# Kernel tuning notes

Hardware: AMD Instinct MI355X
Metric: run time of the kernel (lower is better)

## Reference

```python
import jax, jax.numpy as jnp
import numpy as np

NEG_SLOPE = 0.2  # PyG GATv2 default negative_slope


def _gru_last(x, W_ih, W_hh, b_ih, b_hh):
    """x: [B, T, Hin] -> final GRU hidden state [B, H] (torch nn.GRU equations)."""
    gx = x @ W_ih.T + b_ih  # [B, T, 3H], input gates precomputed
    H = W_hh.shape[1]

    def step(h, g):
        gh = h @ W_hh.T + b_hh
        xr, xz, xn = jnp.split(g, 3, axis=-1)
        hr, hz, hn = jnp.split(gh, 3, axis=-1)
        r = jax.nn.sigmoid(xr + hr)
        z = jax.nn.sigmoid(xz + hz)
        n = jnp.tanh(xn + r * hn)
        return (1.0 - z) * n + z * h, None

    h0 = jnp.zeros((x.shape[0], H), x.dtype)
    hT, _ = jax.lax.scan(step, h0, jnp.swapaxes(gx, 0, 1))
    return hT


def _conv(x, w, b, stride):
    y = jax.lax.conv_general_dilated(x, w, (stride, stride), 'SAME',
                                     dimension_numbers=('NCHW', 'OIHW', 'NCHW'))
    return jax.nn.relu(y + b[None, :, None, None])


def _forward(obs, phase, obs_map, edges, edges_feature, params):
    (W_nbrs, b_nbrs, W_ih, W_hh, b_ih, b_hh, Wl, Wr, att_a, gat_bias,
     conv1_w, conv1_b, conv2_w, conv2_b, Wc, bc, Wp, bp, Wh, bh,
     Wo, bo, Wa, ba) = params
    B, N = obs.shape[0], obs.shape[1]
    BN = B * N
    heads, C = att_a.shape

    # per-node obs embedding (MLP) + GRU over seq -> last hidden
    x = jax.nn.relu(obs.reshape(BN, obs.shape[2], obs.shape[3]) @ W_nbrs + b_nbrs)
    h = _gru_last(x, W_ih, W_hh, b_ih, b_hh)  # [BN, hidden]

    # flat_edges: offset each sample's node ids by b*N, concat along edge dim
    offsets = (jnp.arange(B) * N)[:, None, None]
    ei = (edges + offsets).transpose(1, 0, 2).reshape(2, -1)  # [2, B*E]
    loops = jnp.arange(BN)  # PyG GATv2 add_self_loops=True
    src = jnp.concatenate([ei[0], loops])
    dst = jnp.concatenate([ei[1], loops])

    # GATv2Conv (heads, concat=False): gather -> leakyrelu -> edge softmax -> scatter
    xl = (h @ Wl).reshape(BN, heads, C)
    xr = (h @ Wr).reshape(BN, heads, C)
    e = jax.nn.leaky_relu(xl[src] + xr[dst], NEG_SLOPE)  # [Etot, heads, C]
    logits = jnp.einsum('ehc,hc->eh', e, att_a)          # [Etot, heads]
    m = jax.ops.segment_max(logits, dst, num_segments=BN)
    p = jnp.exp(logits - m[dst])
    s = jax.ops.segment_sum(p, dst, num_segments=BN)
    alpha = p / s[dst]                                    # [Etot, heads]
    node_out = jax.ops.segment_sum(xl[src] * alpha[..., None], dst, num_segments=BN)
    obs_gat = node_out.mean(axis=1) + gat_bias            # concat=False -> head mean

    source_idx = jnp.arange(B) * N  # ego intersection of each sample
    obs_gat = obs_gat[source_idx]   # [B, hidden]

    # CNNBase on map
    c = _conv(obs_map, conv1_w, conv1_b, 2)
    c = _conv(c, conv2_w, conv2_b, 2)
    target_emb = jax.nn.relu(c.reshape(B, -1) @ Wc + bc)

    # phase MLP, fusion MLP, dueling head
    phase_emb = jax.nn.relu(phase @ Wp + bp)
    fused = jnp.concatenate([obs_gat, target_emb, phase_emb], axis=1)
    hid = jax.nn.relu(fused @ Wh + bh)
    v = hid @ Wo + bo
    adv = hid @ Wa + ba
    out = v + (adv - adv.mean(axis=-1, keepdims=True))
    return out, alpha


def setup_inputs() -> dict:
    key = jax.random.key(0)
    B, N, T, Fo = 16, 1000, 16, 16      # batch, n_nodes, seq_len, obs_length+4
    H, heads, P, A, E = 128, 5, 8, 8, 4000
    Cm, HW = 4, 32
    ks = iter(jax.random.split(key, 40))

    def rn(shape, scale=0.05):
        return jax.random.normal(next(ks), shape, dtype=jnp.float32) * scale

    return dict(
        obs=rn((B, N, T, Fo), 1.0),
        phase=rn((B, P), 1.0),
        obs_map=rn((B, Cm, HW, HW), 1.0),
        edges=jax.random.randint(next(ks), (B, 2, E), 0, N),
        edges_feature=rn((B, E, 4), 1.0),
        W_nbrs=rn((Fo, H)), b_nbrs=jnp.zeros((H,), jnp.float32),
        W_ih=rn((3 * H, H)), W_hh=rn((3 * H, H)),
        b_ih=jnp.zeros((3 * H,), jnp.float32), b_hh=jnp.zeros((3 * H,), jnp.float32),
        Wl=rn((H, heads * H)), Wr=rn((H, heads * H)),
        att_a=rn((heads, H)), gat_bias=jnp.zeros((H,), jnp.float32),
        conv1_w=rn((32, Cm, 3, 3)), conv1_b=jnp.zeros((32,), jnp.float32),
        conv2_w=rn((64, 32, 3, 3)), conv2_b=jnp.zeros((64,), jnp.float32),
        Wc=rn((64 * (HW // 4) * (HW // 4), H)), bc=jnp.zeros((H,), jnp.float32),
        Wp=rn((P, P)), bp=jnp.zeros((P,), jnp.float32),
        Wh=rn((2 * H + P, H)), bh=jnp.zeros((H,), jnp.float32),
        Wo=rn((H, 1)), bo=jnp.zeros((1,), jnp.float32),
        Wa=rn((H, A)), ba=jnp.zeros((A,), jnp.float32),
    )


def reference(obs, phase, obs_map, edges, edges_feature,
              W_nbrs, b_nbrs, W_ih, W_hh, b_ih, b_hh,
              Wl, Wr, att_a, gat_bias,
              conv1_w, conv1_b, conv2_w, conv2_b, Wc, bc,
              Wp, bp, Wh, bh, Wo, bo, Wa, ba):
    params = (W_nbrs, b_nbrs, W_ih, W_hh, b_ih, b_hh, Wl, Wr, att_a, gat_bias,
              conv1_w, conv1_b, conv2_w, conv2_b, Wc, bc, Wp, bp, Wh, bh,
              Wo, bo, Wa, ba)
    return _forward(obs, phase, obs_map, edges, edges_feature, params)
```

## Files before the change

### kernel.cpp

```cpp
#include <hip/hip_runtime.h>
#include <hip/hip_bf16.h>
#include <math.h>

#define B_    16
#define N_    1000
#define BN_   16000
#define T_    16
#define FO    16
#define H_    128
#define G3    384
#define HEADS 5
#define HC    640
#define E_    4000
#define EG    64000
#define ETOT  80000
#define P_    8
#define A_    8
#define NEG_SLOPE 0.2f

typedef __attribute__((ext_vector_type(8))) short bf16x8;
typedef __attribute__((ext_vector_type(4))) float f32x4;

__device__ __forceinline__ float bf2f(unsigned short u){ return __uint_as_float(((unsigned)u)<<16); }
__device__ __forceinline__ unsigned short f2bf(float x){
    unsigned u = __float_as_uint(x);
    unsigned r = (u + 0x7FFFu + ((u>>16)&1u)) >> 16;
    return (unsigned short)r;
}
__device__ __forceinline__ unsigned cvtpk(float lo, float hi){
    unsigned r;
    asm volatile("v_cvt_pk_bf16_f32 %0, %1, %2" : "=v"(r) : "v"(lo), "v"(hi));
    return r;
}
__device__ __forceinline__ float rcpf(float x){ return __builtin_amdgcn_rcpf(x); }

__global__ __launch_bounds__(256) void k_prep_c1(
        const float* __restrict__ Wih, const float* __restrict__ Whh,
        const float* __restrict__ Wl, const float* __restrict__ Wr,
        const float* __restrict__ Wn, const float* __restrict__ bn,
        unsigned short* __restrict__ Wihb, unsigned short* __restrict__ Whhb,
        unsigned short* __restrict__ WTb, unsigned short* __restrict__ WnTb,
        float* __restrict__ segsum, float* __restrict__ node_out,
        float* __restrict__ tacc,
        const float* __restrict__ im, const float* __restrict__ w1,
        const float* __restrict__ b1, float* __restrict__ c1out){
    __shared__ float sW[32*4*9];
    int t = threadIdx.x;
    if(blockIdx.x < 640){
        int i = blockIdx.x*256 + t;
        if(i < G3*H_){ Wihb[i] = f2bf(Wih[i]); Whhb[i] = f2bf(Whh[i]); }
        if(i < 2*HC*H_){
            int c = i >> 7, k = i & 127;
            float v = (c < HC) ? Wl[(size_t)k*HC + c] : Wr[(size_t)k*HC + (c-HC)];
            WTb[i] = f2bf(v);
        }
        if(i < H_*32){
            int c = i >> 5, k = i & 31;
            WnTb[i] = (k < FO) ? f2bf(Wn[k*H_ + c])
                     : (k == FO ? f2bf(bn[c]) : (unsigned short)0);
        }
        if(i < BN_*HEADS) segsum[i] = 0.0f;
        if(i < B_*HC) node_out[i] = 0.0f;
        if(i < B_*H_) tacc[i] = 0.0f;
    } else {
        for(int i=t;i<32*4*9;i+=256) sW[i]=w1[i];
        __syncthreads();
        int idx = (blockIdx.x-640)*256 + t;
        int ox = idx & 15, oy = (idx>>4)&15, oc = (idx>>8)&31, b = idx>>13;
        float acc = b1[oc];
        for(int ic=0;ic<4;ic++){
            const float* ip = &im[(size_t)((b*4+ic)*32)*32];
            const float* wp = &sW[(oc*4+ic)*9];
            #pragma unroll
            for(int ky=0;ky<3;ky++){
                int iy = oy*2+ky; if(iy>=32) continue;
                #pragma unroll
                for(int kx=0;kx<3;kx++){
                    int ix = ox*2+kx; if(ix>=32) continue;
                    acc = fmaf(ip[iy*32+ix], wp[ky*3+kx], acc);
                }
            }
        }
        c1out[idx] = fmaxf(acc, 0.f);
    }
}

__global__ __launch_bounds__(512,2) void k_gruf(const float* __restrict__ obs,
        const unsigned short* __restrict__ WnTb,
        const unsigned short* __restrict__ Wihb, const float* __restrict__ bih,
        const unsigned short* __restrict__ Whhb, const float* __restrict__ bhh,
        unsigned short* __restrict__ hout){
    __shared__ unsigned short sX[2*8192];
    __shared__ unsigned short sH[2*8192];
    int t = threadIdx.x;
    int w = t>>6, lane = t&63, lq = lane>>4, lm = lane&15;

    bf16x8 wfi[3][4], wfh[3][4];
    #pragma unroll
    for(int i=0;i<3;i++){
        int row = (8*i + w)*16 + lm;
        #pragma unroll
        for(int kt=0;kt<4;kt++){
            wfi[i][kt] = *(const bf16x8*)&Wihb[row*H_ + kt*32 + lq*8];
            wfh[i][kt] = *(const bf16x8*)&Whhb[row*H_ + kt*32 + lq*8];
        }
    }
    bf16x8 wfn = *(const bf16x8*)&WnTb[(w*16+lm)*32 + lq*8];
    int cb = w*16 + lq*4;
    f32x4 b_r, b_z, bxn, bhn;
    { f32x4 t1=*(const f32x4*)&bih[cb],     t2=*(const f32x4*)&bhh[cb];     b_r=t1+t2; }
    { f32x4 t1=*(const f32x4*)&bih[128+cb], t2=*(const f32x4*)&bhh[128+cb]; b_z=t1+t2; }
    bxn = *(const f32x4*)&bih[256+cb];
    bhn = *(const f32x4*)&bhh[256+cb];

    int rd[4];
    #pragma unroll
    for(int kt=0;kt<4;kt++) rd[kt] = lm*128 + (((4*kt+lq)^(lm&7))<<3);
    const int wrt = lm*128 + (((2*w + (lq>>1))^(lm&7))<<3) + ((lq&1)<<2);

    int nodeBase = blockIdx.x*64;
    const float* obp0 = &obs[(size_t)(nodeBase + lm)*256 + lq*8];

    for(int i=t;i<4096;i+=512) ((unsigned*)sH)[i] = 0u;
    float ho[4][4] = {{0.f,0.f,0.f,0.f},{0.f,0.f,0.f,0.f},
                      {0.f,0.f,0.f,0.f},{0.f,0.f,0.f,0.f}};

    float4 oA[4], oB[4];
    if(lq < 2){
        #pragma unroll
        for(int g=0; g<4; g++){
            const float* q = obp0 + (size_t)g*16*256;
            oA[g] = *(const float4*)(q);    oB[g] = *(const float4*)(q+4);
        }
    }
    #pragma unroll
    for(int g=0; g<4; g++){
        bf16x8 ob = (bf16x8){0,0,0,0,0,0,0,0};
        if(lq < 2){
            union { uint4 u; bf16x8 v; } cv;
            cv.u = make_uint4(cvtpk(oA[g].x,oA[g].y), cvtpk(oA[g].z,oA[g].w),
                              cvtpk(oB[g].x,oB[g].y), cvtpk(oB[g].z,oB[g].w));
            ob = cv.v;
        } else if(lq == 2){
            ob[0] = (short)0x3F80;
        }
        f32x4 xa = (f32x4){0.f,0.f,0.f,0.f};
        xa = __builtin_amdgcn_mfma_f32_16x16x32_bf16(wfn, ob, xa, 0,0,0);
        unsigned u0 = cvtpk(fmaxf(xa[0],0.f), fmaxf(xa[1],0.f));
        unsigned u1 = cvtpk(fmaxf(xa[2],0.f), fmaxf(xa[3],0.f));
        *(uint2*)&sX[g*2048 + wrt] = make_uint2(u0,u1);
    }
    __syncthreads();

    int p = 0;
    #pragma unroll 1
    for(int s=0; s<T_; s++){
        if(s < T_-1 && lq < 2){
            #pragma unroll
            for(int g=0; g<4; g++){
                const float* q = obp0 + (size_t)g*16*256 + (s+1)*16;
                oA[g] = *(const float4*)(q);    oB[g] = *(const float4*)(q+4);
            }
        }
        #pragma unroll
        for(int g=0; g<4; g++){
            int base = p*8192 + g*2048;
            bf16x8 xb[4], hb[4];
            #pragma unroll
            for(int kt=0;kt<4;kt++){
                xb[kt] = *(const bf16x8*)&sX[base + rd[kt]];
                hb[kt] = *(const bf16x8*)&sH[base + rd[kt]];
            }
            f32x4 ar = b_r, az = b_z, axi = bxn, ahh = bhn;
            #pragma unroll
            for(int kt=0;kt<4;kt++){
                ar  = __builtin_amdgcn_mfma_f32_16x16x32_bf16(wfi[0][kt], xb[kt], ar, 0,0,0);
                az  = __builtin_amdgcn_mfma_f32_16x16x32_bf16(wfi[1][kt], xb[kt], az, 0,0,0);
                axi = __builtin_amdgcn_mfma_f32_16x16x32_bf16(wfi[2][kt], xb[kt], axi, 0,0,0);
                ar  = __builtin_amdgcn_mfma_f32_16x16x32_bf16(wfh[0][kt], hb[kt], ar, 0,0,0);
                az  = __builtin_amdgcn_mfma_f32_16x16x32_bf16(wfh[1][kt], hb[kt], az, 0,0,0);
                ahh = __builtin_amdgcn_mfma_f32_16x16x32_bf16(wfh[2][kt], hb[kt], ahh, 0,0,0);
            }
            #pragma unroll
            for(int v=0;v<4;v++){
                float er = __expf(-ar[v]);
                float r  = rcpf(1.f + er);
                float ez = __expf(-az[v]);
                float z  = rcpf(1.f + ez);
                float xn = fmaf(r, ahh[v], axi[v]);
                float en = __expf(-2.f*xn);
                float nn = fmaf(2.f, rcpf(1.f + en), -1.f);
                ho[g][v] = nn + z*(ho[g][v] - nn);
            }
            unsigned u0 = cvtpk(ho[g][0], ho[g][1]);
            unsigned u1 = cvtpk(ho[g][2], ho[g][3]);
            *(uint2*)&sH[(p^1)*8192 + g*2048 + wrt] = make_uint2(u0,u1);
        }
        if(s < T_-1){
            #pragma unroll
            for(int g=0; g<4; g++){
                bf16x8 ob = (bf16x8){0,0,0,0,0,0,0,0};
                if(lq < 2){
                    union { uint4 u; bf16x8 v; } cv;
                    cv.u = make_uint4(cvtpk(oA[g].x,oA[g].y), cvtpk(oA[g].z,oA[g].w),
                                      cvtpk(oB[g].x,oB[g].y), cvtpk(oB[g].z,oB[g].w));
                    ob = cv.v;
                } else if(lq == 2){
                    ob[0] = (short)0x3F80;
                }
                f32x4 xa = (f32x4){0.f,0.f,0.f,0.f};
                xa = __builtin_amdgcn_mfma_f32_16x16x32_bf16(wfn, ob, xa, 0,0,0);
                unsigned u0 = cvtpk(fmaxf(xa[0],0.f), fmaxf(xa[1],0.f));
                unsigned u1 = cvtpk(fmaxf(xa[2],0.f), fmaxf(xa[3],0.f));
                *(uint2*)&sX[(p^1)*8192 + g*2048 + wrt] = make_uint2(u0,u1);
            }
        }
        __syncthreads();
        p ^= 1;
    }
    #pragma unroll
    for(int g=0; g<4; g++){
        unsigned u0 = cvtpk(ho[g][0], ho[g][1]);
        unsigned u1 = cvtpk(ho[g][2], ho[g][3]);
        *(uint2*)&hout[(size_t)(nodeBase + g*16 + lm)*H_ + cb] = make_uint2(u0,u1);
    }
}

__global__ __launch_bounds__(256) void k_xlxr_c2(const unsigned short* __restrict__ hb16,
        const unsigned short* __restrict__ WTb,
        unsigned short* __restrict__ xl, unsigned short* __restrict__ xr,
        const float* __restrict__ c1, const float* __restrict__ w2,
        const float* __restrict__ b2, float* __restrict__ c2out){
    int t = threadIdx.x;
    if(blockIdx.x < 625){
        int w = t>>6, lane = t&63, lq = lane>>4, lm = lane&15;
        int nb = blockIdx.x / 5, cgrp = blockIdx.x % 5;
        int nblk = nb*128;
        int ct0 = cgrp*16 + w*4;
        bf16x8 wf[4][4];
        #pragma unroll
        for(int i=0;i<4;i++){
            int row = (ct0+i)*16 + lm;
            #pragma unroll
            for(int kt=0;kt<4;kt++)
                wf[i][kt] = *(const bf16x8*)&WTb[(size_t)row*H_ + kt*32 + lq*8];
        }
        for(int g=0; g<8; g++){
            int node = nblk + g*16 + lm;
            bf16x8 hb[4];
            #pragma unroll
            for(int kt=0;kt<4;kt++)
                hb[kt] = *(const bf16x8*)&hb16[(size_t)node*H_ + kt*32 + lq*8];
            f32x4 acc[4];
            #pragma unroll
            for(int i=0;i<4;i++) acc[i] = (f32x4){0.f,0.f,0.f,0.f};
            #pragma unroll
            for(int kt=0;kt<4;kt++){
                #pragma unroll
                for(int i=0;i<4;i++)
                    acc[i] = __builtin_amdgcn_mfma_f32_16x16x32_bf16(wf[i][kt], hb[kt], acc[i], 0,0,0);
            }
            #pragma unroll
            for(int i=0;i<4;i++){
                int col = (ct0+i)*16 + lq*4;
                ushort4 o;
                o.x=f2bf(acc[i][0]); o.y=f2bf(acc[i][1]); o.z=f2bf(acc[i][2]); o.w=f2bf(acc[i][3]);
                if(col < HC) *(ushort4*)&xl[(size_t)node*HC + col] = o;
                else         *(ushort4*)&xr[(size_t)node*HC + (col-HC)] = o;
            }
        }
    } else {
        int idx = (blockIdx.x-625)*256 + t;
        int ox = idx & 7, oy = (idx>>3)&7, oc = (idx>>6)&63, b = idx>>12;
        float acc = b2[oc];
        for(int ic=0;ic<32;ic++){
            const float* ip = &c1[(size_t)((b*32+ic)*16)*16];
            const float* wp = &w2[(oc*32+ic)*9];
            #pragma unroll
            for(int ky=0;ky<3;ky++){
                int iy = oy*2+ky; if(iy>=16) continue;
                #pragma unroll
                for(int kx=0;kx<3;kx++){
                    int ix = ox*2+kx; if(ix>=16) continue;
                    acc = fmaf(ip[iy*16+ix], wp[ky*3+kx], acc);
                }
            }
        }
        c2out[idx] = fmaxf(acc, 0.f);
    }
}

__device__ __forceinline__ void edge_sd(int e, const int* __restrict__ edges, int* src, int* dst){
    if(e < EG){
        int b = e / E_, j = e - b*E_;
        *src = edges[(b*2+0)*E_ + j] + b*N_;
        *dst = edges[(b*2+1)*E_ + j] + b*N_;
    } else { *src = *dst = e - EG; }
}

__global__ __launch_bounds__(256) void k_logits_tb(const unsigned short* __restrict__ xl,
        const unsigned short* __restrict__ xr, const int* __restrict__ edges,
        const float* __restrict__ atta, float* __restrict__ pbuf,
        float* __restrict__ segsum,
        const float* __restrict__ c2, const float* __restrict__ Wc,
        float* __restrict__ tacc){
    __shared__ float sC[128];
    int t = threadIdx.x;
    if(blockIdx.x < 5000){
        int lb = (blockIdx.x & 7)*625 + (blockIdx.x >> 3);
        int lane = t & 63, w = t >> 6;
        float am[8], a4[8];
        #pragma unroll
        for(int j=0;j<8;j++) am[j] = atta[lane*8+j];
        #pragma unroll
        for(int j=0;j<8;j++) a4[j] = (lane<16) ? atta[512+lane*8+j] : 0.f;

        int e0 = lb*16 + w*4;
        int srcs[4], dsts[4];
        #pragma unroll
        for(int i=0;i<4;i++) edge_sd(e0+i, edges, &srcs[i], &dsts[i]);
        #pragma unroll
        for(int i=0;i<4;i++){
            const unsigned short* xls = &xl[(size_t)srcs[i]*HC];
            const unsigned short* xrd = &xr[(size_t)dsts[i]*HC];
            uint4 ul = *(const uint4*)&xls[lane*8];
            uint4 ur = *(const uint4*)&xrd[lane*8];
            uint4 tl = make_uint4(0,0,0,0), tr = make_uint4(0,0,0,0);
            if(lane < 16){
                tl = *(const uint4*)&xls[512+lane*8];
                tr = *(const uint4*)&xrd[512+lane*8];
            }
            float pm = 0.f, p4 = 0.f;
            {
                unsigned pl[4] = {ul.x,ul.y,ul.z,ul.w};
                unsigned pr[4] = {ur.x,ur.y,ur.z,ur.w};
                #pragma unroll
                for(int q=0;q<4;q++){
                    float s0 = bf2f((unsigned short)(pl[q]&0xFFFFu)) + bf2f((unsigned short)(pr[q]&0xFFFFu));
                    float s1 = bf2f((unsigned short)(pl[q]>>16))     + bf2f((unsigned short)(pr[q]>>16));
                    s0 = s0 > 0.f ? s0 : NEG_SLOPE*s0;
                    s1 = s1 > 0.f ? s1 : NEG_SLOPE*s1;
                    pm = fmaf(s0, am[2*q],   pm);
                    pm = fmaf(s1, am[2*q+1], pm);
                }
            }
            {
                unsigned ql[4] = {tl.x,tl.y,tl.z,tl.w};
                unsigned qr[4] = {tr.x,tr.y,tr.z,tr.w};
                #pragma unroll
                for(int q=0;q<4;q++){
                    float s0 = bf2f((unsigned short)(ql[q]&0xFFFFu)) + bf2f((unsigned short)(qr[q]&0xFFFFu));
                    float s1 = bf2f((unsigned short)(ql[q]>>16))     + bf2f((unsigned short)(qr[q]>>16));
                    s0 = s0 > 0.f ? s0 : NEG_SLOPE*s0;
                    s1 = s1 > 0.f ? s1 : NEG_SLOPE*s1;
                    p4 = fmaf(s0, a4[2*q],   p4);
                    p4 = fmaf(s1, a4[2*q+1], p4);
                }
            }
            #pragma unroll
            for(int off=1; off<16; off<<=1){
                pm += __shfl_xor(pm, off);
                p4 += __shfl_xor(p4, off);
            }
            if((lane & 15) == 0){
                int hh = lane >> 4;
                float p = __expf(pm);
                pbuf[(size_t)(e0+i)*HEADS + hh] = p;
                atomicAdd(&segsum[dsts[i]*HEADS + hh], p);
            }
            if(lane == 8){
                float p = __expf(p4);
                pbuf[(size_t)(e0+i)*HEADS + 4] = p;
                atomicAdd(&segsum[dsts[i]*HEADS + 4], p);
            }
        }
    } else {
        int bb = blockIdx.x - 5000;
        int b = bb >> 5, ks = bb & 31;
        int k0 = ks*128;
        if(t < 128) sC[t] = c2[(size_t)b*4096 + k0 + t];
        __syncthreads();
        int j = t & 127, sub = t >> 7;
        const float* wp = &Wc[(size_t)(k0 + sub*64)*H_ + j];
        const float* cp = &sC[sub*64];
        float a0=0.f, a1=0.f, a2=0.f, a3=0.f;
        #pragma unroll
        for(int kk=0; kk<64; kk+=4){
            a0 = fmaf(cp[kk+0], wp[(size_t)(kk+0)*H_], a0);
            a1 = fmaf(cp[kk+1], wp[(size_t)(kk+1)*H_], a1);
            a2 = fmaf(cp[kk+2], wp[(size_t)(kk+2)*H_], a2);
            a3 = fmaf(cp[kk+3], wp[(size_t)(kk+3)*H_], a3);
        }
        atomicAdd(&tacc[b*H_+j], (a0+a1)+(a2+a3));
    }
}

__global__ void k_alpha(const float* __restrict__ pbuf, const float* __restrict__ segsum,
                        const int* __restrict__ edges, const unsigned short* __restrict__ xl,
                        float* __restrict__ out_alpha, float* __restrict__ node_out){
    int idx = blockIdx.x*256 + threadIdx.x;
    int lane = threadIdx.x & 63;
    bool valid = idx < ETOT*HEADS;
    int e = 0, hh = 0, src = 0, dst = 0;
    float a = 0.f;
    bool ego = false;
    if(valid){
        e = idx / HEADS; hh = idx - e*HEADS;
        edge_sd(e, edges, &src, &dst);
        a = pbuf[idx] / segsum[dst*HEADS + hh];
        out_alpha[idx] = a;
        ego = (dst % N_) == 0;
    }
    unsigned long long m = __ballot(ego);
    while(m){
        int l = __ffsll((unsigned long long)m) - 1;
        m &= (m - 1);
        float aa = __shfl(a, l);
        int ss = __shfl(src, l), dd = __shfl(dst, l), hq = __shfl(hh, l);
        int b = dd / N_;
        unsigned u = *(const unsigned*)&xl[(size_t)ss*HC + hq*H_ + lane*2];
        float* no = &node_out[b*HC + hq*H_ + lane*2];
        atomicAdd(no,     aa * bf2f((unsigned short)(u & 0xFFFFu)));
        atomicAdd(no + 1, aa * bf2f((unsigned short)(u >> 16)));
    }
}

__global__ __launch_bounds__(256) void k_head(const float* __restrict__ node_out,
        const float* __restrict__ gat_bias, const float* __restrict__ tacc,
        const float* __restrict__ bc, const float* __restrict__ phase,
        const float* __restrict__ Wp, const float* __restrict__ bp,
        const float* __restrict__ Wh, const float* __restrict__ bh,
        const float* __restrict__ Wo, const float* __restrict__ bo,
        const float* __restrict__ Wa, const float* __restrict__ ba,
        float* __restrict__ out){
    __shared__ float sF[16][268];
    __shared__ float sHid[16][132];
    int t = threadIdx.x;
    for(int i=t;i<B_*H_;i+=256){
        int b=i>>7, c=i&127;
        float s=0.f;
        #pragma unroll
        for(int hh=0;hh<HEADS;hh++) s += node_out[b*HC + hh*H_ + c];
        sF[b][c] = s*(1.0f/HEADS) + gat_bias[c];
    }
    for(int i=t;i<B_*H_;i+=256){
        int b=i>>7, c=i&127;
        sF[b][128+c] = fmaxf(tacc[i] + bc[c], 0.f);
    }
    if(t < B_*P_){
        int b=t>>3, p=t&7;
        float s=bp[p];
        #pragma unroll
        for(int q=0;q<P_;q++) s = fmaf(phase[b*P_+q], Wp[q*P_+p], s);
        sF[b][256+p] = fmaxf(s, 0.f);
    }
    __syncthreads();
    for(int i=t;i<B_*H_;i+=256){
        int b=i>>7, j=i&127;
        float s=bh[j];
        for(int k=0;k<2*H_+P_;k++) s = fmaf(sF[b][k], Wh[k*H_+j], s);
        sHid[b][j]=fmaxf(s,0.f);
    }
    __syncthreads();
    if(t < B_*A_){
        int b=t>>3, a=t&7;
        float v=bo[0], ad=ba[a];
        for(int k=0;k<H_;k++){ float hv=sHid[b][k]; v = fmaf(hv,Wo[k],v); ad = fmaf(hv,Wa[k*A_+a],ad); }
        float m = ad;
        m += __shfl_xor(m,1); m += __shfl_xor(m,2); m += __shfl_xor(m,4);
        m *= 0.125f;
        out[b*A_+a] = v + ad - m;
    }
}

extern "C" void kernel_launch(void* const* d_in, const int* in_sizes, int n_in,
                              void* d_out, int out_size, void* d_ws, size_t ws_size,
                              hipStream_t stream) {
    (void)in_sizes; (void)n_in; (void)out_size; (void)ws_size;
    const float* obs      = (const float*)d_in[0];
    const float* phase    = (const float*)d_in[1];
    const float* obs_map  = (const float*)d_in[2];
    const int*   edges    = (const int*)  d_in[3];
    const float* W_nbrs   = (const float*)d_in[5];
    const float* b_nbrs   = (const float*)d_in[6];
    const float* W_ih     = (const float*)d_in[7];
    const float* W_hh     = (const float*)d_in[8];
    const float* b_ih     = (const float*)d_in[9];
    const float* b_hh     = (const float*)d_in[10];
    const float* Wl       = (const float*)d_in[11];
    const float* Wr       = (const float*)d_in[12];
    const float* att_a    = (const float*)d_in[13];
    const float* gat_bias = (const float*)d_in[14];
    const float* conv1_w  = (const float*)d_in[15];
    const float* conv1_b  = (const float*)d_in[16];
    const float* conv2_w  = (const float*)d_in[17];
    const float* conv2_b  = (const float*)d_in[18];
    const float* Wc       = (const float*)d_in[19];
    const float* bc       = (const float*)d_in[20];
    const float* Wp       = (const float*)d_in[21];
    const float* bp       = (const float*)d_in[22];
    const float* Wh       = (const float*)d_in[23];
    const float* bh       = (const float*)d_in[24];
    const float* Wo       = (const float*)d_in[25];
    const float* bo       = (const float*)d_in[26];
    const float* Wa       = (const float*)d_in[27];
    const float* ba       = (const float*)d_in[28];

    float* out = (float*)d_out;
    float* w   = (float*)d_ws;

    size_t off = 0;
    unsigned short* hbuf = (unsigned short*)(w + off); off += (size_t)BN_*H_/2;
    unsigned short* xl   = (unsigned short*)(w + off); off += (size_t)BN_*HC/2;
    unsigned short* xr   = (unsigned short*)(w + off); off += (size_t)BN_*HC/2;
    float* pbuf   = w + off; off += (size_t)ETOT*HEADS;
    float* segsum = w + off; off += (size_t)BN_*HEADS;
    float* nodeo  = w + off; off += (size_t)B_*HC;
    float* c1     = w + off; off += (size_t)16*32*16*16;
    float* c2     = w + off; off += (size_t)16*64*8*8;
    float* tacc   = w + off; off += (size_t)B_*H_;
    unsigned short* Wihb = (unsigned short*)(w + off); off += (size_t)H_*G3/2;
    unsigned short* Whhb = (unsigned short*)(w + off); off += (size_t)H_*G3/2;
    unsigned short* WTb  = (unsigned short*)(w + off); off += (size_t)2*HC*H_/2;
    unsigned short* WnTb = (unsigned short*)(w + off); off += (size_t)H_*32/2;

    k_prep_c1<<<640 + 512, 256, 0, stream>>>(W_ih, W_hh, Wl, Wr, W_nbrs, b_nbrs,
                                             Wihb, Whhb, WTb, WnTb,
                                             segsum, nodeo, tacc,
                                             obs_map, conv1_w, conv1_b, c1);

    k_gruf<<<BN_/64, 512, 0, stream>>>(obs, WnTb, Wihb, b_ih, Whhb, b_hh, hbuf);

    k_xlxr_c2<<<625 + 256, 256, 0, stream>>>(hbuf, WTb, xl, xr,
                                             c1, conv2_w, conv2_b, c2);

    k_logits_tb<<<5000 + 512, 256, 0, stream>>>(xl, xr, edges, att_a, pbuf, segsum,
                                                c2, Wc, tacc);

    k_alpha<<<(ETOT*HEADS+255)/256, 256, 0, stream>>>(pbuf, segsum, edges, xl, out+128, nodeo);

    k_head<<<1, 256, 0, stream>>>(nodeo, gat_bias, tacc, bc, phase,
                                  Wp, bp, Wh, bh, Wo, bo, Wa, ba, out);
}
```

Measured before the change: 199.1 us.

## Fold log2e scaling into GRU weights and interleave two node groups in MFMA chain

Pre-scales the r/z gate weights and biases by log2(e) and the n-gate ones by 2·log2(e), so the GRU activations can use exp2f directly instead of __expf with negation and scaling. The per-step loop now handles two 16-node groups at a time with interleaved independent MFMA accumulators, which hides MFMA dependency latency. The obs prefetch held in registers across the whole step is replaced by loads issued just before the input projection, which lowers register pressure but exposes global load latency. The r·hn term now uses the pre-scaled hn, which is consistent with the scaled xn, though the bf16 rounding of the scaled weights changes numerics slightly.

```diff
diff --git a/kernel.cpp b/kernel.cpp
--- a/kernel.cpp
+++ b/kernel.cpp
@@ -17,6 +17,7 @@
 #define P_    8
 #define A_    8
 #define NEG_SLOPE 0.2f
+#define L2E   1.44269504f
 
 typedef __attribute__((ext_vector_type(8))) short bf16x8;
 typedef __attribute__((ext_vector_type(4))) float f32x4;
@@ -48,7 +49,10 @@
     int t = threadIdx.x;
     if(blockIdx.x < 640){
         int i = blockIdx.x*256 + t;
-        if(i < G3*H_){ Wihb[i] = f2bf(Wih[i]); Whhb[i] = f2bf(Whh[i]); }
+        if(i < G3*H_){
+            float sc = ((i >> 7) < 256) ? L2E : 2.0f*L2E;
+            Wihb[i] = f2bf(Wih[i]*sc); Whhb[i] = f2bf(Whh[i]*sc);
+        }
         if(i < 2*HC*H_){
             int c = i >> 7, k = i & 127;
             float v = (c < HC) ? Wl[(size_t)k*HC + c] : Wr[(size_t)k*HC + (c-HC)];
@@ -108,10 +112,10 @@
     bf16x8 wfn = *(const bf16x8*)&WnTb[(w*16+lm)*32 + lq*8];
     int cb = w*16 + lq*4;
     f32x4 b_r, b_z, bxn, bhn;
-    { f32x4 t1=*(const f32x4*)&bih[cb],     t2=*(const f32x4*)&bhh[cb];     b_r=t1+t2; }
-    { f32x4 t1=*(const f32x4*)&bih[128+cb], t2=*(const f32x4*)&bhh[128+cb]; b_z=t1+t2; }
-    bxn = *(const f32x4*)&bih[256+cb];
-    bhn = *(const f32x4*)&bhh[256+cb];
+    { f32x4 t1=*(const f32x4*)&bih[cb],     t2=*(const f32x4*)&bhh[cb];     b_r=(t1+t2)*L2E; }
+    { f32x4 t1=*(const f32x4*)&bih[128+cb], t2=*(const f32x4*)&bhh[128+cb]; b_z=(t1+t2)*L2E; }
+    bxn = *(const f32x4*)&bih[256+cb] * (2.0f*L2E);
+    bhn = *(const f32x4*)&bhh[256+cb] * (2.0f*L2E);
 
     int rd[4];
     #pragma unroll
@@ -125,21 +129,15 @@
     float ho[4][4] = {{0.f,0.f,0.f,0.f},{0.f,0.f,0.f,0.f},
                       {0.f,0.f,0.f,0.f},{0.f,0.f,0.f,0.f}};
 
-    float4 oA[4], oB[4];
-    if(lq < 2){
-        #pragma unroll
-        for(int g=0; g<4; g++){
-            const float* q = obp0 + (size_t)g*16*256;
-            oA[g] = *(const float4*)(q);    oB[g] = *(const float4*)(q+4);
-        }
-    }
     #pragma unroll
     for(int g=0; g<4; g++){
         bf16x8 ob = (bf16x8){0,0,0,0,0,0,0,0};
         if(lq < 2){
+            const float* q = obp0 + (size_t)g*16*256;
+            float4 a = *(const float4*)(q), b = *(const float4*)(q+4);
             union { uint4 u; bf16x8 v; } cv;
-            cv.u = make_uint4(cvtpk(oA[g].x,oA[g].y), cvtpk(oA[g].z,oA[g].w),
-                              cvtpk(oB[g].x,oB[g].y), cvtpk(oB[g].z,oB[g].w));
+            cv.u = make_uint4(cvtpk(a.x,a.y), cvtpk(a.z,a.w),
+                              cvtpk(b.x,b.y), cvtpk(b.z,b.w));
             ob = cv.v;
         } else if(lq == 2){
             ob[0] = (short)0x3F80;
@@ -155,64 +153,77 @@
     int p = 0;
     #pragma unroll 1
     for(int s=0; s<T_; s++){
-        if(s < T_-1 && lq < 2){
-            #pragma unroll
-            for(int g=0; g<4; g++){
-                const float* q = obp0 + (size_t)g*16*256 + (s+1)*16;
-                oA[g] = *(const float4*)(q);    oB[g] = *(const float4*)(q+4);
-            }
-        }
-        #pragma unroll
-        for(int g=0; g<4; g++){
-            int base = p*8192 + g*2048;
-            bf16x8 xb[4], hb[4];
+        #pragma unroll
+        for(int pr=0; pr<2; pr++){
+            int g0 = pr*2, g1 = pr*2+1;
+            int base0 = p*8192 + g0*2048;
+            int base1 = p*8192 + g1*2048;
+            bf16x8 xb0[4], hb0[4], xb1[4], hb1[4];
             #pragma unroll
             for(int kt=0;kt<4;kt++){
-                xb[kt] = *(const bf16x8*)&sX[base + rd[kt]];
-                hb[kt] = *(const bf16x8*)&sH[base + rd[kt]];
-            }
-            f32x4 ar = b_r, az = b_z, axi = bxn, ahh = bhn;
+                xb0[kt] = *(const bf16x8*)&sX[base0 + rd[kt]];
+                hb0[kt] = *(const bf16x8*)&sH[base0 + rd[kt]];
+                xb1[kt] = *(const bf16x8*)&sX[base1 + rd[kt]];
+                hb1[kt] = *(const bf16x8*)&sH[base1 + rd[kt]];
+            }
+            f32x4 ar0=b_r, az0=b_z, ax0=bxn, ah0=bhn;
+            f32x4 ar1=b_r, az1=b_z, ax1=bxn, ah1=bhn;
             #pragma unroll
             for(int kt=0;kt<4;kt++){
-                ar  = __builtin_amdgcn_mfma_f32_16x16x32_bf16(wfi[0][kt], xb[kt], ar, 0,0,0);
-                az  = __builtin_amdgcn_mfma_f32_16x16x32_bf16(wfi[1][kt], xb[kt], az, 0,0,0);
-                axi = __builtin_amdgcn_mfma_f32_16x16x32_bf16(wfi[2][kt], xb[kt], axi, 0,0,0);
-                ar  = __builtin_amdgcn_mfma_f32_16x16x32_bf16(wfh[0][kt], hb[kt], ar, 0,0,0);
-                az  = __builtin_amdgcn_mfma_f32_16x16x32_bf16(wfh[1][kt], hb[kt], az, 0,0,0);
-                ahh = __builtin_amdgcn_mfma_f32_16x16x32_bf16(wfh[2][kt], hb[kt], ahh, 0,0,0);
+                ar0 = __builtin_amdgcn_mfma_f32_16x16x32_bf16(wfi[0][kt], xb0[kt], ar0, 0,0,0);
+                ar1 = __builtin_amdgcn_mfma_f32_16x16x32_bf16(wfi[0][kt], xb1[kt], ar1, 0,0,0);
+                az0 = __builtin_amdgcn_mfma_f32_16x16x32_bf16(wfi[1][kt], xb0[kt], az0, 0,0,0);
+                az1 = __builtin_amdgcn_mfma_f32_16x16x32_bf16(wfi[1][kt], xb1[kt], az1, 0,0,0);
+                ax0 = __builtin_amdgcn_mfma_f32_16x16x32_bf16(wfi[2][kt], xb0[kt], ax0, 0,0,0);
+                ax1 = __builtin_amdgcn_mfma_f32_16x16x32_bf16(wfi[2][kt], xb1[kt], ax1, 0,0,0);
+                ar0 = __builtin_amdgcn_mfma_f32_16x16x32_bf16(wfh[0][kt], hb0[kt], ar0, 0,0,0);
+                ar1 = __builtin_amdgcn_mfma_f32_16x16x32_bf16(wfh[0][kt], hb1[kt], ar1, 0,0,0);
+                az0 = __builtin_amdgcn_mfma_f32_16x16x32_bf16(wfh[1][kt], hb0[kt], az0, 0,0,0);
+                az1 = __builtin_amdgcn_mfma_f32_16x16x32_bf16(wfh[1][kt], hb1[kt], az1, 0,0,0);
+                ah0 = __builtin_amdgcn_mfma_f32_16x16x32_bf16(wfh[2][kt], hb0[kt], ah0, 0,0,0);
+                ah1 = __builtin_amdgcn_mfma_f32_16x16x32_bf16(wfh[2][kt], hb1[kt], ah1, 0,0,0);
             }
             #pragma unroll
             for(int v=0;v<4;v++){
-                float er = __expf(-ar[v]);
-                float r  = rcpf(1.f + er);
-                float ez = __expf(-az[v]);
-                float z  = rcpf(1.f + ez);
-                float xn = fmaf(r, ahh[v], axi[v]);
-                float en = __expf(-2.f*xn);
-                float nn = fmaf(2.f, rcpf(1.f + en), -1.f);
-                ho[g][v] = nn + z*(ho[g][v] - nn);
-            }
-            unsigned u0 = cvtpk(ho[g][0], ho[g][1]);
-            unsigned u1 = cvtpk(ho[g][2], ho[g][3]);
-            *(uint2*)&sH[(p^1)*8192 + g*2048 + wrt] = make_uint2(u0,u1);
-        }
-        if(s < T_-1){
-            #pragma unroll
-            for(int g=0; g<4; g++){
-                bf16x8 ob = (bf16x8){0,0,0,0,0,0,0,0};
-                if(lq < 2){
-                    union { uint4 u; bf16x8 v; } cv;
-                    cv.u = make_uint4(cvtpk(oA[g].x,oA[g].y), cvtpk(oA[g].z,oA[g].w),
-                                      cvtpk(oB[g].x,oB[g].y), cvtpk(oB[g].z,oB[g].w));
-                    ob = cv.v;
-                } else if(lq == 2){
-                    ob[0] = (short)0x3F80;
+                float r  = rcpf(1.f + exp2f(-ar0[v]));
+                float z  = rcpf(1.f + exp2f(-az0[v]));
+                float xn = fmaf(r, ah0[v], ax0[v]);
+                float nn = fmaf(2.f, rcpf(1.f + exp2f(-xn)), -1.f);
+                ho[g0][v] = nn + z*(ho[g0][v] - nn);
+            }
+            #pragma unroll
+            for(int v=0;v<4;v++){
+                float r  = rcpf(1.f + exp2f(-ar1[v]));
+                float z  = rcpf(1.f + exp2f(-az1[v]));
+                float xn = fmaf(r, ah1[v], ax1[v]);
+                float nn = fmaf(2.f, rcpf(1.f + exp2f(-xn)), -1.f);
+                ho[g1][v] = nn + z*(ho[g1][v] - nn);
+            }
+            *(uint2*)&sH[(p^1)*8192 + g0*2048 + wrt] =
+                make_uint2(cvtpk(ho[g0][0], ho[g0][1]), cvtpk(ho[g0][2], ho[g0][3]));
+            *(uint2*)&sH[(p^1)*8192 + g1*2048 + wrt] =
+                make_uint2(cvtpk(ho[g1][0], ho[g1][1]), cvtpk(ho[g1][2], ho[g1][3]));
+            if(s < T_-1){
+                #pragma unroll
+                for(int gi=0; gi<2; gi++){
+                    int g = pr*2 + gi;
+                    bf16x8 ob = (bf16x8){0,0,0,0,0,0,0,0};
+                    if(lq < 2){
+                        const float* q = obp0 + (size_t)g*16*256 + (s+1)*16;
+                        float4 a = *(const float4*)(q), b = *(const float4*)(q+4);
+                        union { uint4 u; bf16x8 v; } cv;
+                        cv.u = make_uint4(cvtpk(a.x,a.y), cvtpk(a.z,a.w),
+                                          cvtpk(b.x,b.y), cvtpk(b.z,b.w));
+                        ob = cv.v;
+                    } else if(lq == 2){
+                        ob[0] = (short)0x3F80;
+                    }
+                    f32x4 xa = (f32x4){0.f,0.f,0.f,0.f};
+                    xa = __builtin_amdgcn_mfma_f32_16x16x32_bf16(wfn, ob, xa, 0,0,0);
+                    unsigned u0 = cvtpk(fmaxf(xa[0],0.f), fmaxf(xa[1],0.f));
+                    unsigned u1 = cvtpk(fmaxf(xa[2],0.f), fmaxf(xa[3],0.f));
+                    *(uint2*)&sX[(p^1)*8192 + g*2048 + wrt] = make_uint2(u0,u1);
                 }
-                f32x4 xa = (f32x4){0.f,0.f,0.f,0.f};
-                xa = __builtin_amdgcn_mfma_f32_16x16x32_bf16(wfn, ob, xa, 0,0,0);
-                unsigned u0 = cvtpk(fmaxf(xa[0],0.f), fmaxf(xa[1],0.f));
-                unsigned u1 = cvtpk(fmaxf(xa[2],0.f), fmaxf(xa[3],0.f));
-                *(uint2*)&sX[(p^1)*8192 + g*2048 + wrt] = make_uint2(u0,u1);
             }
         }
         __syncthreads();
```

Measured after the change: 203.0 us. Within noise of the previous version (+2.0%).
